# Performance work log

Measured on AMD Instinct MI355X. Metric: run time of the kernel, lower is better.

## Reference

```python
import jax, jax.numpy as jnp
import numpy as np

EMB = 1024
HEADS = 16
HEAD_DIM = EMB // HEADS
B, S = 4, 2048


def setup_inputs() -> dict:
    key = jax.random.key(0)
    ks = jax.random.split(key, 7)
    sc = 1.0 / np.sqrt(EMB)
    return {
        "query": jax.random.normal(ks[0], (B, S, EMB), jnp.float32),
        "key": jax.random.normal(ks[1], (B, S, EMB), jnp.float32),
        "value": jax.random.normal(ks[2], (B, S, EMB), jnp.float32),
        "Wq": jax.random.normal(ks[3], (EMB, EMB), jnp.float32) * sc,
        "Wk": jax.random.normal(ks[4], (EMB, EMB), jnp.float32) * sc,
        "Wv": jax.random.normal(ks[5], (EMB, EMB), jnp.float32) * sc,
        "Wo": jax.random.normal(ks[6], (EMB, EMB), jnp.float32) * sc,
    }


def reference(query, key, value, Wq, Wk, Wv, Wo):
    # nn.Linear applies x @ W^T; W stored as [out, in]
    def split_heads(x):  # [B,S,E] -> [B,H,S,D]
        return x.reshape(B, -1, HEADS, HEAD_DIM).transpose(0, 2, 1, 3)

    q = split_heads(query @ Wq.T)
    k = split_heads(key @ Wk.T)
    v = split_heads(value @ Wv.T)
    scores = jnp.einsum('bhse,bhte->bhst', q, k) / np.sqrt(HEAD_DIM).astype(np.float32)
    attn = jax.nn.softmax(scores, axis=-1)
    ctx = jnp.einsum('bhst,bhtd->bshd', attn, v)  # [B,S,H,D]
    out = ctx.reshape(B, -1, EMB) @ Wo.T
    return out
```

## Files before the change

### kernel.cpp

```cpp
#include <hip/hip_runtime.h>
#include <hip/hip_bf16.h>

#define EMB   1024
#define HEADS 16
#define HDIM  64
#define BB    4
#define SS    2048
#define MROWS (BB*SS)

typedef __bf16 bf16_t;
typedef __bf16 bf16x4_t __attribute__((ext_vector_type(4)));
typedef __bf16 bf16x8   __attribute__((ext_vector_type(8)));
typedef float  f32x4    __attribute__((ext_vector_type(4)));

__device__ __forceinline__ void glds16(const void* g, void* l) {
  __builtin_amdgcn_global_load_lds(
      (const __attribute__((address_space(1))) void*)g,
      (__attribute__((address_space(3))) void*)l, 16, 0, 0);
}

__launch_bounds__(256)
__global__ void cast_multi(const float* s0, const float* s1, const float* s2,
                           const float* s3, const float* s4, const float* s5,
                           const float* s6,
                           bf16_t* d0, bf16_t* d1, bf16_t* d2, bf16_t* d3,
                           bf16_t* d4, bf16_t* d5, bf16_t* d6, int nact) {
  const int z = blockIdx.z;
  if (z >= nact && blockIdx.x >= 512) return;
  const float* ss[7] = {s0, s1, s2, s3, s4, s5, s6};
  bf16_t*      dd[7] = {d0, d1, d2, d3, d4, d5, d6};
  const float* s = ss[z];
  bf16_t*      d = dd[z];
  const int i = (blockIdx.x*256 + threadIdx.x) * 8;
  const f32x4 a = *(const f32x4*)&s[i];
  const f32x4 b = *(const f32x4*)&s[i+4];
  bf16x8 r;
  r[0]=(bf16_t)a[0]; r[1]=(bf16_t)a[1]; r[2]=(bf16_t)a[2]; r[3]=(bf16_t)a[3];
  r[4]=(bf16_t)b[0]; r[5]=(bf16_t)b[1]; r[6]=(bf16_t)b[2]; r[7]=(bf16_t)b[3];
  *(bf16x8*)&d[i] = r;
}

__launch_bounds__(256)
__global__ void cast_f32_bf16(const float* __restrict__ src, bf16_t* __restrict__ dst) {
  const int i = (blockIdx.x*256 + threadIdx.x) * 8;
  const f32x4 a = *(const f32x4*)&src[i];
  const f32x4 b = *(const f32x4*)&src[i+4];
  bf16x8 r;
  r[0]=(bf16_t)a[0]; r[1]=(bf16_t)a[1]; r[2]=(bf16_t)a[2]; r[3]=(bf16_t)a[3];
  r[4]=(bf16_t)b[0]; r[5]=(bf16_t)b[1]; r[6]=(bf16_t)b[2]; r[7]=(bf16_t)b[3];
  *(bf16x8*)&dst[i] = r;
}

__device__ __forceinline__ void gemm_core(const bf16_t* __restrict__ A,
                                          const bf16_t* __restrict__ W,
                                          bf16_t* As, bf16_t* Bs,
                                          f32x4 acc[4][4],
                                          int bm0, int bn0,
                                          int wave, int lane) {
  const int quad = lane >> 4, l16 = lane & 15;
  const int wm = wave >> 1, wn = wave & 1;
  for (int k0 = 0; k0 < EMB; k0 += 32) {
#pragma unroll
    for (int j = 0; j < 2; ++j) {
      const int i   = wave*2 + j;
      const int row = i*16 + (lane >> 2);
      const int col = (lane & 3) * 8;
      glds16(A + (size_t)(bm0 + row)*EMB + k0 + col, &As[i*512]);
      glds16(W + (size_t)(bn0 + row)*EMB + k0 + col, &Bs[i*512]);
    }
    __syncthreads();

    bf16x8 a[4], b[4];
#pragma unroll
    for (int t = 0; t < 4; ++t) {
      a[t] = *(const bf16x8*)&As[(wm*64 + t*16 + l16)*32 + quad*8];
      b[t] = *(const bf16x8*)&Bs[(wn*64 + t*16 + l16)*32 + quad*8];
    }
#pragma unroll
    for (int mt = 0; mt < 4; ++mt)
#pragma unroll
      for (int nt = 0; nt < 4; ++nt)
        acc[mt][nt] = __builtin_amdgcn_mfma_f32_16x16x32_bf16(a[mt], b[nt], acc[mt][nt], 0, 0, 0);
    __syncthreads();
  }
}

__launch_bounds__(256)
__global__ void gemm_qkv(const bf16_t* A0, const bf16_t* A1, const bf16_t* A2,
                         const bf16_t* W0, const bf16_t* W1, const bf16_t* W2,
                         bf16_t* C0, bf16_t* C1, bf16_t* C2,
                         float sscale, int zbase) {
  __shared__ __align__(16) bf16_t As[128*32];
  __shared__ __align__(16) bf16_t Bs[128*32];
  const int tid  = threadIdx.x;
  const int wave = tid >> 6, lane = tid & 63;
  const int quad = lane >> 4, l16 = lane & 15;
  const int wm = wave >> 1, wn = wave & 1;

  const int fid = blockIdx.x + 8*(blockIdx.y + 64*blockIdx.z);
  const int xcd = fid & 7, s = fid >> 3;
  const int bn0 = (s & 7) * 128;
  const int p   = xcd + 8*(s >> 3);
  const int z   = (p >> 6) + zbase;
  const int bm0 = (p & 63) * 128;

  const bf16_t* A = (z == 0) ? A0 : (z == 1) ? A1 : A2;
  const bf16_t* W = (z == 0) ? W0 : (z == 1) ? W1 : W2;
  bf16_t*       C = (z == 0) ? C0 : (z == 1) ? C1 : C2;
  const float oscale = (z == 0) ? sscale : 1.0f;

  f32x4 acc[4][4] = {};
  gemm_core(A, W, As, Bs, acc, bm0, bn0, wave, lane);

  if (z == 2) {
    const int bb = bm0 >> 11;
    const int T  = ((bm0 & 2047) >> 6) + wm;
    const int h  = (bn0 >> 6) + wn;
    bf16_t* base = C + ((size_t)(bb*HEADS + h)*32 + T)*4096;
#pragma unroll
    for (int ks = 0; ks < 2; ++ks)
#pragma unroll
      for (int nt = 0; nt < 4; ++nt) {
        bf16x8 v;
#pragma unroll
        for (int r = 0; r < 4; ++r) {
          v[r]     = (bf16_t)acc[2*ks][nt][r];
          v[4 + r] = (bf16_t)acc[2*ks + 1][nt][r];
        }
        *(bf16x8*)&base[((nt*2 + ks)*64 + quad*16 + l16)*8] = v;
      }
  } else {
#pragma unroll
    for (int mt = 0; mt < 4; ++mt) {
      const int row = bm0 + wm*64 + mt*16 + quad*4;
#pragma unroll
      for (int nt = 0; nt < 4; ++nt) {
        const int col = bn0 + wn*64 + nt*16 + l16;
#pragma unroll
        for (int r = 0; r < 4; ++r)
          C[(size_t)(row + r)*EMB + col] = (bf16_t)(acc[mt][nt][r] * oscale);
      }
    }
  }
}

__launch_bounds__(256)
__global__ void gemm_out(const bf16_t* __restrict__ A, const bf16_t* __restrict__ W,
                         float* __restrict__ C) {
  __shared__ __align__(16) bf16_t As[128*32];
  __shared__ __align__(16) bf16_t Bs[128*32];
  const int tid  = threadIdx.x;
  const int wave = tid >> 6, lane = tid & 63;
  const int quad = lane >> 4, l16 = lane & 15;
  const int wm = wave >> 1, wn = wave & 1;

  const int fid = blockIdx.x + 8*blockIdx.y;
  const int xcd = fid & 7, s = fid >> 3;
  const int bn0 = (s & 7) * 128;
  const int bm0 = (xcd*8 + (s >> 3)) * 128;

  f32x4 acc[4][4] = {};
  gemm_core(A, W, As, Bs, acc, bm0, bn0, wave, lane);

#pragma unroll
  for (int mt = 0; mt < 4; ++mt) {
    const int row = bm0 + wm*64 + mt*16 + quad*4;
#pragma unroll
    for (int nt = 0; nt < 4; ++nt) {
      const int col = bn0 + wn*64 + nt*16 + l16;
#pragma unroll
      for (int r = 0; r < 4; ++r)
        C[(size_t)(row + r)*EMB + col] = acc[mt][nt][r];
    }
  }
}

__launch_bounds__(512, 8)
__global__ void attn(const bf16_t* Qp, const bf16_t* __restrict__ Kp,
                     const bf16_t* __restrict__ Vt, bf16_t* Cx) {
  __shared__ __align__(16) bf16_t Ks[2][4096];
  __shared__ __align__(16) bf16_t Vs[2][4096];

  const int tid  = threadIdx.x;
  const int wave = tid >> 6, lane = tid & 63;
  const int quad = lane >> 4, l16 = lane & 15;

  const int fid  = blockIdx.x + 16*(blockIdx.y + 16*blockIdx.z);
  const int xcd  = fid & 7, s = fid >> 3;
  const int q0   = (s & 15) * 128;
  const int pair = xcd*8 + (s >> 4);
  const int h    = pair & 15;
  const int b    = pair >> 4;

  bf16x8 qf[2];
  {
    const size_t qr = (size_t)(b*SS + q0 + wave*16 + l16)*EMB + h*HDIM;
    qf[0] = *(const bf16x8*)&Qp[qr + quad*8];
    qf[1] = *(const bf16x8*)&Qp[qr + 32 + quad*8];
  }

  const bf16_t* Kb = Kp + (size_t)b*SS*EMB + h*HDIM;
  const bf16_t* Vb = Vt + ((size_t)(b*HEADS + h)*32)*4096;

  f32x4 o[4] = {};
  f32x4 lsv = {};

  auto stage = [&](int ti, int bf) {
    const int t0 = ti * 64;
    const int i  = wave;
    glds16(Kb + (size_t)(t0 + (i&3)*16 + l16)*EMB + (i>>2)*32 + quad*8,
           &Ks[bf][i*512]);
    glds16(Vb + (size_t)ti*4096 + i*512 + lane*8, &Vs[bf][i*512]);
  };

  stage(0, 0);

  const int NT = SS / 64;
  for (int t = 0, buf = 0; t < NT; ++t, buf ^= 1) {
    __syncthreads();
    if (t + 1 < NT) stage(t + 1, buf ^ 1);

    f32x4 st[4] = {};
#pragma unroll
    for (int cb = 0; cb < 4; ++cb) {
      const bf16x8 kf0 = *(const bf16x8*)&Ks[buf][cb*512 + lane*8];
      const bf16x8 kf1 = *(const bf16x8*)&Ks[buf][2048 + cb*512 + lane*8];
      st[cb] = __builtin_amdgcn_mfma_f32_16x16x32_bf16(kf0, qf[0], st[cb], 0, 0, 0);
      st[cb] = __builtin_amdgcn_mfma_f32_16x16x32_bf16(kf1, qf[1], st[cb], 0, 0, 0);
    }

#pragma unroll
    for (int kb = 0; kb < 4; ++kb) {
#pragma unroll
      for (int r = 0; r < 4; ++r)
        st[kb][r] = __builtin_amdgcn_exp2f(st[kb][r]);
      lsv += st[kb];
    }
    bf16x8 pb[2];
#pragma unroll
    for (int ks = 0; ks < 2; ++ks)
#pragma unroll
      for (int r = 0; r < 4; ++r) {
        pb[ks][r]     = (bf16_t)st[2*ks][r];
        pb[ks][4 + r] = (bf16_t)st[2*ks + 1][r];
      }

#pragma unroll
    for (int ks = 0; ks < 2; ++ks)
#pragma unroll
      for (int dt = 0; dt < 4; ++dt) {
        const bf16x8 vf = *(const bf16x8*)&Vs[buf][((dt*2 + ks)*64 + lane)*8];
        o[dt] = __builtin_amdgcn_mfma_f32_16x16x32_bf16(vf, pb[ks], o[dt], 0, 0, 0);
      }
  }

  float l = lsv[0] + lsv[1] + lsv[2] + lsv[3];
  l += __shfl_xor(l, 16, 64);
  l += __shfl_xor(l, 32, 64);
  const float inv = 1.0f / l;
  const size_t row = (size_t)(b*SS + q0 + wave*16 + l16)*EMB + h*HDIM;
#pragma unroll
  for (int dt = 0; dt < 4; ++dt) {
    bf16x4_t v;
#pragma unroll
    for (int r = 0; r < 4; ++r) v[r] = (bf16_t)(o[dt][r] * inv);
    *(bf16x4_t*)&Cx[row + dt*16 + quad*4] = v;
  }
}

extern "C" void kernel_launch(void* const* d_in, const int* in_sizes, int n_in,
                              void* d_out, int out_size, void* d_ws, size_t ws_size,
                              hipStream_t stream) {
  (void)in_sizes; (void)n_in; (void)out_size;
  const float* query = (const float*)d_in[0];
  const float* key   = (const float*)d_in[1];
  const float* value = (const float*)d_in[2];
  const float* WqF   = (const float*)d_in[3];
  const float* WkF   = (const float*)d_in[4];
  const float* WvF   = (const float*)d_in[5];
  const float* WoF   = (const float*)d_in[6];

  const size_t AN = (size_t)MROWS*EMB;
  const size_t WN = (size_t)EMB*EMB;
  float* out = (float*)d_out;
  bf16_t* S5 = (bf16_t*)d_out;
  bf16_t* S6 = S5 + AN;

  const float sscale = 0.125f * 1.44269504f;

  const dim3 gqkv(EMB/128, MROWS/128, 3);
  const dim3 gqk (EMB/128, MROWS/128, 2);
  const dim3 gv  (EMB/128, MROWS/128, 1);
  const dim3 gg  (EMB/128, MROWS/128);
  const dim3 gattn(SS/128, HEADS, BB);

  if (ws_size >= (size_t)(4*AN + 4*WN) * sizeof(bf16_t)) {
    bf16_t* qb  = (bf16_t*)d_ws;
    bf16_t* kb  = qb + AN;
    bf16_t* vb  = kb + AN;
    bf16_t* S2  = vb + AN;
    bf16_t* Wqb = S2 + AN;
    bf16_t* Wkb = Wqb + WN;
    bf16_t* Wvb = Wkb + WN;
    bf16_t* Wob = Wvb + WN;

    cast_multi<<<dim3(AN/2048, 1, 7), 256, 0, stream>>>(
        query, key, value, WqF, WkF, WvF, WoF,
        qb, kb, vb, Wqb, Wkb, Wvb, Wob, 3);
    gemm_qkv<<<gqkv, 256, 0, stream>>>(qb, kb, vb, Wqb, Wkb, Wvb,
                                       S2, S6, S5, sscale, 0);
    attn<<<gattn, 512, 0, stream>>>(S2, S6, S5, S2);
    gemm_out<<<gg, 256, 0, stream>>>(S2, Wob, out);
  } else {
    bf16_t* S1  = (bf16_t*)d_ws;
    bf16_t* S2  = S1 + AN;
    bf16_t* Wqb = S2 + AN;
    bf16_t* Wkb = Wqb + WN;
    bf16_t* Wvb = Wkb + WN;
    bf16_t* Wob = Wvb + WN;

    cast_multi<<<dim3(AN/2048, 1, 6), 256, 0, stream>>>(
        query, key, WqF, WkF, WvF, WoF, WoF,
        S1, S5, Wqb, Wkb, Wvb, Wob, Wob, 2);
    gemm_qkv<<<gqk, 256, 0, stream>>>(S1, S5, S1, Wqb, Wkb, Wvb,
                                      S2, S6, S5, sscale, 0);
    cast_f32_bf16<<<dim3(AN/2048), 256, 0, stream>>>(value, S1);
    gemm_qkv<<<gv, 256, 0, stream>>>(S1, S1, S1, Wvb, Wvb, Wvb,
                                     S5, S5, S5, 1.0f, 2);
    attn<<<gattn, 512, 0, stream>>>(S2, S6, S5, S2);
    gemm_out<<<gg, 256, 0, stream>>>(S2, Wob, out);
  }
}
```

Baseline: 325.3 us.

## Fuse fp32-to-bf16 activation cast into double-buffered QKV GEMM

The QKV projection GEMM now reads the fp32 query/key/value directly, converts to bf16 in registers and writes the result into LDS. This removes the separate activation cast pass and its bf16 round trip through global memory. The GEMM is also double-buffered, prefetching the next K-tile while computing the current one. Only the weights are still cast in a separate kernel. Each A tile now costs twice as many fp32 bytes from global memory, and register use goes up.

```diff
diff --git a/kernel.cpp b/kernel.cpp
--- a/kernel.cpp
+++ b/kernel.cpp
@@ -20,15 +20,12 @@
 }
 
 __launch_bounds__(256)
-__global__ void cast_multi(const float* s0, const float* s1, const float* s2,
-                           const float* s3, const float* s4, const float* s5,
-                           const float* s6,
-                           bf16_t* d0, bf16_t* d1, bf16_t* d2, bf16_t* d3,
-                           bf16_t* d4, bf16_t* d5, bf16_t* d6, int nact) {
+__global__ void cast_w(const float* s0, const float* s1, const float* s2,
+                       const float* s3,
+                       bf16_t* d0, bf16_t* d1, bf16_t* d2, bf16_t* d3) {
   const int z = blockIdx.z;
-  if (z >= nact && blockIdx.x >= 512) return;
-  const float* ss[7] = {s0, s1, s2, s3, s4, s5, s6};
-  bf16_t*      dd[7] = {d0, d1, d2, d3, d4, d5, d6};
+  const float* ss[4] = {s0, s1, s2, s3};
+  bf16_t*      dd[4] = {d0, d1, d2, d3};
   const float* s = ss[z];
   bf16_t*      d = dd[z];
   const int i = (blockIdx.x*256 + threadIdx.x) * 8;
@@ -40,15 +37,121 @@
   *(bf16x8*)&d[i] = r;
 }
 
-__launch_bounds__(256)
-__global__ void cast_f32_bf16(const float* __restrict__ src, bf16_t* __restrict__ dst) {
-  const int i = (blockIdx.x*256 + threadIdx.x) * 8;
-  const f32x4 a = *(const f32x4*)&src[i];
-  const f32x4 b = *(const f32x4*)&src[i+4];
-  bf16x8 r;
-  r[0]=(bf16_t)a[0]; r[1]=(bf16_t)a[1]; r[2]=(bf16_t)a[2]; r[3]=(bf16_t)a[3];
-  r[4]=(bf16_t)b[0]; r[5]=(bf16_t)b[1]; r[6]=(bf16_t)b[2]; r[7]=(bf16_t)b[3];
-  *(bf16x8*)&dst[i] = r;
+__launch_bounds__(256, 4)
+__global__ void gemm_qkv(const float* A0, const float* A1, const float* A2,
+                         const bf16_t* W0, const bf16_t* W1, const bf16_t* W2,
+                         bf16_t* C0, bf16_t* C1, bf16_t* C2, float sscale) {
+  __shared__ __align__(16) bf16_t As[2][4096];
+  __shared__ __align__(16) bf16_t Bs[2][4096];
+  const int tid  = threadIdx.x;
+  const int wave = tid >> 6, lane = tid & 63;
+  const int quad = lane >> 4, l16 = lane & 15;
+  const int wm = wave >> 1, wn = wave & 1;
+
+  const int fid = blockIdx.x + 8*(blockIdx.y + 64*blockIdx.z);
+  const int xcd = fid & 7, s = fid >> 3;
+  const int bn0 = (s & 7) * 128;
+  const int p   = xcd + 8*(s >> 3);
+  const int z   = p >> 6;
+  const int bm0 = (p & 63) * 128;
+
+  const float*  A = (z == 0) ? A0 : (z == 1) ? A1 : A2;
+  const bf16_t* W = (z == 0) ? W0 : (z == 1) ? W1 : W2;
+  bf16_t*       C = (z == 0) ? C0 : (z == 1) ? C1 : C2;
+  const float oscale = (z == 0) ? sscale : 1.0f;
+
+  const int arow  = tid >> 1;
+  const int acolh = (tid & 1) * 16;
+  const float* Arow = A + (size_t)(bm0 + arow)*EMB + acolh;
+
+  f32x4 acc[4][4] = {};
+  f32x4 ar[4];
+
+  auto loadA = [&](int k0) {
+#pragma unroll
+    for (int j = 0; j < 4; ++j)
+      ar[j] = *(const f32x4*)&Arow[k0 + j*4];
+  };
+  auto writeA = [&](int bf) {
+    bf16x8 h0, h1;
+#pragma unroll
+    for (int r = 0; r < 4; ++r) {
+      h0[r] = (bf16_t)ar[0][r];  h0[4+r] = (bf16_t)ar[1][r];
+      h1[r] = (bf16_t)ar[2][r];  h1[4+r] = (bf16_t)ar[3][r];
+    }
+    *(bf16x8*)&As[bf][arow*32 + acolh]     = h0;
+    *(bf16x8*)&As[bf][arow*32 + acolh + 8] = h1;
+  };
+  auto stageW = [&](int k0, int bf) {
+#pragma unroll
+    for (int j = 0; j < 2; ++j) {
+      const int i   = wave*2 + j;
+      const int row = i*16 + (lane >> 2);
+      const int col = (lane & 3) * 8;
+      glds16(W + (size_t)(bn0 + row)*EMB + k0 + col, &Bs[bf][i*512]);
+    }
+  };
+  auto compute = [&](int bf) {
+    bf16x8 a[4], b[4];
+#pragma unroll
+    for (int t2 = 0; t2 < 4; ++t2) {
+      a[t2] = *(const bf16x8*)&As[bf][(wm*64 + t2*16 + l16)*32 + quad*8];
+      b[t2] = *(const bf16x8*)&Bs[bf][(wn*64 + t2*16 + l16)*32 + quad*8];
+    }
+#pragma unroll
+    for (int mt = 0; mt < 4; ++mt)
+#pragma unroll
+      for (int nt = 0; nt < 4; ++nt)
+        acc[mt][nt] = __builtin_amdgcn_mfma_f32_16x16x32_bf16(a[mt], b[nt], acc[mt][nt], 0, 0, 0);
+  };
+
+  loadA(0);
+  stageW(0, 0);
+  writeA(0);
+  __syncthreads();
+
+  const int NK = EMB / 32;
+  for (int t = 0; t < NK; ++t) {
+    const int cur = t & 1;
+    if (t + 1 < NK) {
+      loadA((t + 1) * 32);
+      stageW((t + 1) * 32, cur ^ 1);
+    }
+    compute(cur);
+    if (t + 1 < NK) writeA(cur ^ 1);
+    __syncthreads();
+  }
+
+  if (z == 2) {
+    const int bb = bm0 >> 11;
+    const int T  = ((bm0 & 2047) >> 6) + wm;
+    const int h  = (bn0 >> 6) + wn;
+    bf16_t* base = C + ((size_t)(bb*HEADS + h)*32 + T)*4096;
+#pragma unroll
+    for (int ks = 0; ks < 2; ++ks)
+#pragma unroll
+      for (int nt = 0; nt < 4; ++nt) {
+        bf16x8 v;
+#pragma unroll
+        for (int r = 0; r < 4; ++r) {
+          v[r]     = (bf16_t)acc[2*ks][nt][r];
+          v[4 + r] = (bf16_t)acc[2*ks + 1][nt][r];
+        }
+        *(bf16x8*)&base[((nt*2 + ks)*64 + quad*16 + l16)*8] = v;
+      }
+  } else {
+#pragma unroll
+    for (int mt = 0; mt < 4; ++mt) {
+      const int row = bm0 + wm*64 + mt*16 + quad*4;
+#pragma unroll
+      for (int nt = 0; nt < 4; ++nt) {
+        const int col = bn0 + wn*64 + nt*16 + l16;
+#pragma unroll
+        for (int r = 0; r < 4; ++r)
+          C[(size_t)(row + r)*EMB + col] = (bf16_t)(acc[mt][nt][r] * oscale);
+      }
+    }
+  }
 }
 
 __device__ __forceinline__ void gemm_core(const bf16_t* __restrict__ A,
@@ -86,65 +189,6 @@
 }
 
 __launch_bounds__(256)
-__global__ void gemm_qkv(const bf16_t* A0, const bf16_t* A1, const bf16_t* A2,
-                         const bf16_t* W0, const bf16_t* W1, const bf16_t* W2,
-                         bf16_t* C0, bf16_t* C1, bf16_t* C2,
-                         float sscale, int zbase) {
-  __shared__ __align__(16) bf16_t As[128*32];
-  __shared__ __align__(16) bf16_t Bs[128*32];
-  const int tid  = threadIdx.x;
-  const int wave = tid >> 6, lane = tid & 63;
-  const int quad = lane >> 4, l16 = lane & 15;
-  const int wm = wave >> 1, wn = wave & 1;
-
-  const int fid = blockIdx.x + 8*(blockIdx.y + 64*blockIdx.z);
-  const int xcd = fid & 7, s = fid >> 3;
-  const int bn0 = (s & 7) * 128;
-  const int p   = xcd + 8*(s >> 3);
-  const int z   = (p >> 6) + zbase;
-  const int bm0 = (p & 63) * 128;
-
-  const bf16_t* A = (z == 0) ? A0 : (z == 1) ? A1 : A2;
-  const bf16_t* W = (z == 0) ? W0 : (z == 1) ? W1 : W2;
-  bf16_t*       C = (z == 0) ? C0 : (z == 1) ? C1 : C2;
-  const float oscale = (z == 0) ? sscale : 1.0f;
-
-  f32x4 acc[4][4] = {};
-  gemm_core(A, W, As, Bs, acc, bm0, bn0, wave, lane);
-
-  if (z == 2) {
-    const int bb = bm0 >> 11;
-    const int T  = ((bm0 & 2047) >> 6) + wm;
-    const int h  = (bn0 >> 6) + wn;
-    bf16_t* base = C + ((size_t)(bb*HEADS + h)*32 + T)*4096;
-#pragma unroll
-    for (int ks = 0; ks < 2; ++ks)
-#pragma unroll
-      for (int nt = 0; nt < 4; ++nt) {
-        bf16x8 v;
-#pragma unroll
-        for (int r = 0; r < 4; ++r) {
-          v[r]     = (bf16_t)acc[2*ks][nt][r];
-          v[4 + r] = (bf16_t)acc[2*ks + 1][nt][r];
-        }
-        *(bf16x8*)&base[((nt*2 + ks)*64 + quad*16 + l16)*8] = v;
-      }
-  } else {
-#pragma unroll
-    for (int mt = 0; mt < 4; ++mt) {
-      const int row = bm0 + wm*64 + mt*16 + quad*4;
-#pragma unroll
-      for (int nt = 0; nt < 4; ++nt) {
-        const int col = bn0 + wn*64 + nt*16 + l16;
-#pragma unroll
-        for (int r = 0; r < 4; ++r)
-          C[(size_t)(row + r)*EMB + col] = (bf16_t)(acc[mt][nt][r] * oscale);
-      }
-    }
-  }
-}
-
-__launch_bounds__(256)
 __global__ void gemm_out(const bf16_t* __restrict__ A, const bf16_t* __restrict__ W,
                          float* __restrict__ C) {
   __shared__ __align__(16) bf16_t As[128*32];
@@ -271,7 +315,7 @@
 extern "C" void kernel_launch(void* const* d_in, const int* in_sizes, int n_in,
                               void* d_out, int out_size, void* d_ws, size_t ws_size,
                               hipStream_t stream) {
-  (void)in_sizes; (void)n_in; (void)out_size;
+  (void)in_sizes; (void)n_in; (void)out_size; (void)ws_size;
   const float* query = (const float*)d_in[0];
   const float* key   = (const float*)d_in[1];
   const float* value = (const float*)d_in[2];
@@ -286,48 +330,22 @@
   bf16_t* S5 = (bf16_t*)d_out;
   bf16_t* S6 = S5 + AN;
 
+  bf16_t* S2  = (bf16_t*)d_ws;
+  bf16_t* Wqb = S2 + AN;
+  bf16_t* Wkb = Wqb + WN;
+  bf16_t* Wvb = Wkb + WN;
+  bf16_t* Wob = Wvb + WN;
+
   const float sscale = 0.125f * 1.44269504f;
 
+  const dim3 gw  (512, 1, 4);
   const dim3 gqkv(EMB/128, MROWS/128, 3);
-  const dim3 gqk (EMB/128, MROWS/128, 2);
-  const dim3 gv  (EMB/128, MROWS/128, 1);
   const dim3 gg  (EMB/128, MROWS/128);
   const dim3 gattn(SS/128, HEADS, BB);
 
-  if (ws_size >= (size_t)(4*AN + 4*WN) * sizeof(bf16_t)) {
-    bf16_t* qb  = (bf16_t*)d_ws;
-    bf16_t* kb  = qb + AN;
-    bf16_t* vb  = kb + AN;
-    bf16_t* S2  = vb + AN;
-    bf16_t* Wqb = S2 + AN;
-    bf16_t* Wkb = Wqb + WN;
-    bf16_t* Wvb = Wkb + WN;
-    bf16_t* Wob = Wvb + WN;
-
-    cast_multi<<<dim3(AN/2048, 1, 7), 256, 0, stream>>>(
-        query, key, value, WqF, WkF, WvF, WoF,
-        qb, kb, vb, Wqb, Wkb, Wvb, Wob, 3);
-    gemm_qkv<<<gqkv, 256, 0, stream>>>(qb, kb, vb, Wqb, Wkb, Wvb,
-                                       S2, S6, S5, sscale, 0);
-    attn<<<gattn, 512, 0, stream>>>(S2, S6, S5, S2);
-    gemm_out<<<gg, 256, 0, stream>>>(S2, Wob, out);
-  } else {
-    bf16_t* S1  = (bf16_t*)d_ws;
-    bf16_t* S2  = S1 + AN;
-    bf16_t* Wqb = S2 + AN;
-    bf16_t* Wkb = Wqb + WN;
-    bf16_t* Wvb = Wkb + WN;
-    bf16_t* Wob = Wvb + WN;
-
-    cast_multi<<<dim3(AN/2048, 1, 6), 256, 0, stream>>>(
-        query, key, WqF, WkF, WvF, WoF, WoF,
-        S1, S5, Wqb, Wkb, Wvb, Wob, Wob, 2);
-    gemm_qkv<<<gqk, 256, 0, stream>>>(S1, S5, S1, Wqb, Wkb, Wvb,
-                                      S2, S6, S5, sscale, 0);
-    cast_f32_bf16<<<dim3(AN/2048), 256, 0, stream>>>(value, S1);
-    gemm_qkv<<<gv, 256, 0, stream>>>(S1, S1, S1, Wvb, Wvb, Wvb,
-                                     S5, S5, S5, 1.0f, 2);
-    attn<<<gattn, 512, 0, stream>>>(S2, S6, S5, S2);
-    gemm_out<<<gg, 256, 0, stream>>>(S2, Wob, out);
-  }
-}
+  cast_w<<<gw, 256, 0, stream>>>(WqF, WkF, WvF, WoF, Wqb, Wkb, Wvb, Wob);
+  gemm_qkv<<<gqkv, 256, 0, stream>>>(query, key, value, Wqb, Wkb, Wvb,
+                                     S2, S6, S5, sscale);
+  attn<<<gattn, 512, 0, stream>>>(S2, S6, S5, S2);
+  gemm_out<<<gg, 256, 0, stream>>>(S2, Wob, out);
+}
```

After: 345.0 us. +6.0%, slower.

## Double-buffer GEMM LDS tiles and shrink output GEMM M-tile to 64

Applied to the files above, without the earlier changes.

Adds double-buffered shared-memory staging to the GEMM core so the next K-slice's global-to-LDS loads are issued while the current slice is being multiplied, removing one barrier per iteration. The output projection is also rewritten with a 64x128 tile and a grid of 8x128 blocks, doubling the block count to improve CU occupancy and load balance. The trade-off is twice the LDS per block and smaller per-block arithmetic intensity for the output GEMM.

```diff
diff --git a/kernel.cpp b/kernel.cpp
--- a/kernel.cpp
+++ b/kernel.cpp
@@ -53,35 +53,42 @@
 
 __device__ __forceinline__ void gemm_core(const bf16_t* __restrict__ A,
                                           const bf16_t* __restrict__ W,
-                                          bf16_t* As, bf16_t* Bs,
+                                          bf16_t (*As)[4096], bf16_t (*Bs)[4096],
                                           f32x4 acc[4][4],
                                           int bm0, int bn0,
                                           int wave, int lane) {
   const int quad = lane >> 4, l16 = lane & 15;
   const int wm = wave >> 1, wn = wave & 1;
-  for (int k0 = 0; k0 < EMB; k0 += 32) {
+
+  auto stage = [&](int k0, int bf) {
 #pragma unroll
     for (int j = 0; j < 2; ++j) {
       const int i   = wave*2 + j;
       const int row = i*16 + (lane >> 2);
       const int col = (lane & 3) * 8;
-      glds16(A + (size_t)(bm0 + row)*EMB + k0 + col, &As[i*512]);
-      glds16(W + (size_t)(bn0 + row)*EMB + k0 + col, &Bs[i*512]);
-    }
+      glds16(A + (size_t)(bm0 + row)*EMB + k0 + col, &As[bf][i*512]);
+      glds16(W + (size_t)(bn0 + row)*EMB + k0 + col, &Bs[bf][i*512]);
+    }
+  };
+
+  stage(0, 0);
+  const int NK = EMB / 32;
+  for (int t = 0; t < NK; ++t) {
+    const int cur = t & 1;
     __syncthreads();
+    if (t + 1 < NK) stage((t + 1) * 32, cur ^ 1);
 
     bf16x8 a[4], b[4];
 #pragma unroll
-    for (int t = 0; t < 4; ++t) {
-      a[t] = *(const bf16x8*)&As[(wm*64 + t*16 + l16)*32 + quad*8];
-      b[t] = *(const bf16x8*)&Bs[(wn*64 + t*16 + l16)*32 + quad*8];
+    for (int t2 = 0; t2 < 4; ++t2) {
+      a[t2] = *(const bf16x8*)&As[cur][(wm*64 + t2*16 + l16)*32 + quad*8];
+      b[t2] = *(const bf16x8*)&Bs[cur][(wn*64 + t2*16 + l16)*32 + quad*8];
     }
 #pragma unroll
     for (int mt = 0; mt < 4; ++mt)
 #pragma unroll
       for (int nt = 0; nt < 4; ++nt)
         acc[mt][nt] = __builtin_amdgcn_mfma_f32_16x16x32_bf16(a[mt], b[nt], acc[mt][nt], 0, 0, 0);
-    __syncthreads();
   }
 }
 
@@ -90,8 +97,8 @@
                          const bf16_t* W0, const bf16_t* W1, const bf16_t* W2,
                          bf16_t* C0, bf16_t* C1, bf16_t* C2,
                          float sscale, int zbase) {
-  __shared__ __align__(16) bf16_t As[128*32];
-  __shared__ __align__(16) bf16_t Bs[128*32];
+  __shared__ __align__(16) bf16_t As[2][4096];
+  __shared__ __align__(16) bf16_t Bs[2][4096];
   const int tid  = threadIdx.x;
   const int wave = tid >> 6, lane = tid & 63;
   const int quad = lane >> 4, l16 = lane & 15;
@@ -147,8 +154,8 @@
 __launch_bounds__(256)
 __global__ void gemm_out(const bf16_t* __restrict__ A, const bf16_t* __restrict__ W,
                          float* __restrict__ C) {
-  __shared__ __align__(16) bf16_t As[128*32];
-  __shared__ __align__(16) bf16_t Bs[128*32];
+  __shared__ __align__(16) bf16_t As[2][2048];
+  __shared__ __align__(16) bf16_t Bs[2][4096];
   const int tid  = threadIdx.x;
   const int wave = tid >> 6, lane = tid & 63;
   const int quad = lane >> 4, l16 = lane & 15;
@@ -157,14 +164,50 @@
   const int fid = blockIdx.x + 8*blockIdx.y;
   const int xcd = fid & 7, s = fid >> 3;
   const int bn0 = (s & 7) * 128;
-  const int bm0 = (xcd*8 + (s >> 3)) * 128;
-
-  f32x4 acc[4][4] = {};
-  gemm_core(A, W, As, Bs, acc, bm0, bn0, wave, lane);
-
-#pragma unroll
-  for (int mt = 0; mt < 4; ++mt) {
-    const int row = bm0 + wm*64 + mt*16 + quad*4;
+  const int bm0 = (xcd*16 + (s >> 3)) * 64;
+
+  auto stage = [&](int k0, int bf) {
+    {
+      const int i   = wave;
+      const int row = i*16 + (lane >> 2);
+      const int col = (lane & 3) * 8;
+      glds16(A + (size_t)(bm0 + row)*EMB + k0 + col, &As[bf][i*512]);
+    }
+#pragma unroll
+    for (int j = 0; j < 2; ++j) {
+      const int i   = wave*2 + j;
+      const int row = i*16 + (lane >> 2);
+      const int col = (lane & 3) * 8;
+      glds16(W + (size_t)(bn0 + row)*EMB + k0 + col, &Bs[bf][i*512]);
+    }
+  };
+
+  f32x4 acc[2][4] = {};
+
+  stage(0, 0);
+  const int NK = EMB / 32;
+  for (int t = 0; t < NK; ++t) {
+    const int cur = t & 1;
+    __syncthreads();
+    if (t + 1 < NK) stage((t + 1) * 32, cur ^ 1);
+
+    bf16x8 a[2], b[4];
+#pragma unroll
+    for (int t2 = 0; t2 < 2; ++t2)
+      a[t2] = *(const bf16x8*)&As[cur][(wm*32 + t2*16 + l16)*32 + quad*8];
+#pragma unroll
+    for (int t2 = 0; t2 < 4; ++t2)
+      b[t2] = *(const bf16x8*)&Bs[cur][(wn*64 + t2*16 + l16)*32 + quad*8];
+#pragma unroll
+    for (int mt = 0; mt < 2; ++mt)
+#pragma unroll
+      for (int nt = 0; nt < 4; ++nt)
+        acc[mt][nt] = __builtin_amdgcn_mfma_f32_16x16x32_bf16(a[mt], b[nt], acc[mt][nt], 0, 0, 0);
+  }
+
+#pragma unroll
+  for (int mt = 0; mt < 2; ++mt) {
+    const int row = bm0 + wm*32 + mt*16 + quad*4;
 #pragma unroll
     for (int nt = 0; nt < 4; ++nt) {
       const int col = bn0 + wn*64 + nt*16 + l16;
@@ -291,7 +334,7 @@
   const dim3 gqkv(EMB/128, MROWS/128, 3);
   const dim3 gqk (EMB/128, MROWS/128, 2);
   const dim3 gv  (EMB/128, MROWS/128, 1);
-  const dim3 gg  (EMB/128, MROWS/128);
+  const dim3 gg  (8, 128);
   const dim3 gattn(SS/128, HEADS, BB);
 
   if (ws_size >= (size_t)(4*AN + 4*WN) * sizeof(bf16_t)) {
```

Result: slower. 333.0 us (+2.3%).
